# Kernel tuning notes

Measured on AMD Instinct MI355X. Metric: run time of the kernel, lower is better.

## Reference

```python
import jax, jax.numpy as jnp
import numpy as np

WINDOW_SIZE = 11
SIGMA = 1.5
C1 = 0.01 ** 2
C2 = 0.03 ** 2


def _gaussian_window(window_size, channel, dtype):
    coords = jnp.arange(window_size, dtype=jnp.float32) - window_size // 2
    g = jnp.exp(-(coords ** 2) / (2.0 * SIGMA ** 2))
    g = g / g.sum()
    w2d = jnp.outer(g, g)  # [K, K]
    # depthwise kernel: [channel, 1, K, K] (OIHW with feature_group_count=channel)
    return jnp.broadcast_to(w2d, (channel, 1, window_size, window_size)).astype(dtype)


def _dwconv(x, window, channel):
    pad = WINDOW_SIZE // 2
    return jax.lax.conv_general_dilated(
        x, window,
        window_strides=(1, 1),
        padding=[(pad, pad), (pad, pad)],
        dimension_numbers=('NCHW', 'OIHW', 'NCHW'),
        feature_group_count=channel,
    )


def _ssim(img1, img2):
    channel = img1.shape[1]
    window = _gaussian_window(WINDOW_SIZE, channel, img1.dtype)
    mu1 = _dwconv(img1, window, channel)
    mu2 = _dwconv(img2, window, channel)
    mu1_sq = mu1 * mu1
    mu2_sq = mu2 * mu2
    mu1_mu2 = mu1 * mu2
    sigma1_sq = _dwconv(img1 * img1, window, channel) - mu1_sq
    sigma2_sq = _dwconv(img2 * img2, window, channel) - mu2_sq
    sigma12 = _dwconv(img1 * img2, window, channel) - mu1_mu2
    ssim_map = ((2.0 * mu1_mu2 + C1) * (2.0 * sigma12 + C2)) / (
        (mu1_sq + mu2_sq + C1) * (sigma1_sq + sigma2_sq + C2))
    return ssim_map.mean()


def setup_inputs() -> dict:
    key = jax.random.key(0)
    k1, k2 = jax.random.split(key)
    img1 = jax.random.uniform(k1, (32, 3, 512, 512), dtype=jnp.float32)
    img2 = jax.random.uniform(k2, (32, 3, 512, 512), dtype=jnp.float32)
    return {"img1": img1, "img2": img2}


def reference(img1, img2):
    return _ssim(img1, img2)
```

## Files before the change

kernel.cpp:

```cpp
#include <hip/hip_runtime.h>
#include <cmath>

#define IMG_H 512
#define IMG_W 512
#define TH 32
#define TW 64
#define LDSW 75
#define NPLANES 96
#define NPIX 25165824.0

typedef float vf2 __attribute__((ext_vector_type(2)));

struct GaussW { float w[11]; };

__global__ __launch_bounds__(256, 4) void ssim_main(
    const float* __restrict__ img1, const float* __restrict__ img2,
    float* __restrict__ partials, GaussW gw, int use_atomic, float* __restrict__ out)
{
    __shared__ vf2 VAB[TH][LDSW];
    __shared__ vf2 VTS[TH][LDSW];
    __shared__ float wsum[4];

    const int tid = threadIdx.x;
    const int plane = blockIdx.z;
    const int tr0 = blockIdx.y * TH;
    const int tc0 = blockIdx.x * TW;
    const float* __restrict__ plane1 = img1 + ((size_t)plane << 18);
    const float* __restrict__ plane2 = img2 + ((size_t)plane << 18);

    {
        const int j = tid % 80;
        const int chunk = tid / 80;
        if (chunk < 3 && j < 74) {
            const int r0 = chunk * 11;
            const int gc = tc0 + j - 5;
            const float cmask = ((unsigned)gc < IMG_W) ? 1.f : 0.f;
            const int gcc = min(max(gc, 0), IMG_W - 1);

            vf2 aAB[11], aTS[11];

            #pragma unroll
            for (int ii = 0; ii < 21; ++ii) {
                const int gr = tr0 + r0 - 5 + ii;
                const float rmask = ((unsigned)gr < IMG_H) ? cmask : 0.f;
                const int grc = min(max(gr, 0), IMG_H - 1);
                const uint32_t idx = (uint32_t)(grc * IMG_W + gcc);
                const float a = plane1[idx] * rmask;
                const float b = plane2[idx] * rmask;
                const vf2 ab = { a, b };
                const vf2 pq = ab * ab;
                const vf2 ts = { pq.x + pq.y, a * b };
                #pragma unroll
                for (int o = 0; o < 11; ++o) {
                    if (o <= ii && ii <= o + 10) {
                        const float wt = gw.w[ii - o];
                        const vf2 wtv = { wt, wt };
                        if (ii == o) {
                            aAB[o] = wtv * ab;
                            aTS[o] = wtv * ts;
                        } else {
                            aAB[o] = __builtin_elementwise_fma(wtv, ab, aAB[o]);
                            aTS[o] = __builtin_elementwise_fma(wtv, ts, aTS[o]);
                        }
                    }
                }
            }
            #pragma unroll
            for (int o = 0; o < 11; ++o) {
                const int r = r0 + o;
                if (r0 + o < TH) {
                    VAB[r][j] = aAB[o];
                    VTS[r][j] = aTS[o];
                }
            }
        }
    }
    __syncthreads();

    float lsum = 0.f;
    {
        const int r = tid & 31;
        const int c0 = (tid >> 5) * 8;
        const vf2* __restrict__ bAB = &VAB[r][c0];
        const vf2* __restrict__ bTS = &VTS[r][c0];

        vf2 mAB[8], eTS[8];

        #pragma unroll
        for (int k = 0; k <= 17; ++k) {
            const vf2 vab = bAB[k];
            const vf2 vts = bTS[k];
            #pragma unroll
            for (int c = 0; c < 8; ++c) {
                if (k - 10 <= c && c <= k) {
                    const float wt = gw.w[k - c];
                    const vf2 wtv = { wt, wt };
                    if (k == c) {
                        mAB[c] = wtv * vab;
                        eTS[c] = wtv * vts;
                    } else {
                        mAB[c] = __builtin_elementwise_fma(wtv, vab, mAB[c]);
                        eTS[c] = __builtin_elementwise_fma(wtv, vts, eTS[c]);
                    }
                }
            }
        }
        #pragma unroll
        for (int c = 0; c < 8; ++c) {
            const float a1 = mAB[c].x, a2 = mAB[c].y;
            const float T  = eTS[c].x, S = eTS[c].y;
            const float h    = fmaf(a1, a1, a2 * a2);
            const float mu12 = a1 * a2;
            const float num  = fmaf(2.f, mu12, 0.0001f)
                             * fmaf(2.f, S - mu12, 0.0009f);
            const float den  = (h + 0.0001f) * ((T - h) + 0.0009f);
            lsum = fmaf(num, __builtin_amdgcn_rcpf(den), lsum);
        }
    }
    #pragma unroll
    for (int off = 32; off; off >>= 1) lsum += __shfl_down(lsum, off, 64);
    if ((tid & 63) == 0) wsum[tid >> 6] = lsum;
    __syncthreads();
    if (tid == 0) {
        const float bs = wsum[0] + wsum[1] + wsum[2] + wsum[3];
        if (use_atomic) {
            atomicAdd(out, bs * (float)(1.0 / NPIX));
        } else {
            const int bId = (blockIdx.z * gridDim.y + blockIdx.y) * gridDim.x + blockIdx.x;
            partials[bId] = bs;
        }
    }
}

__global__ __launch_bounds__(256) void ssim_reduce(
    const float* __restrict__ partials, int n, float* __restrict__ out)
{
    const int tid = threadIdx.x;
    double s = 0.0;
    for (int i = tid; i < n; i += 256) s += (double)partials[i];
    #pragma unroll
    for (int off = 32; off; off >>= 1) s += __shfl_down(s, off, 64);
    __shared__ double ws[4];
    if ((tid & 63) == 0) ws[tid >> 6] = s;
    __syncthreads();
    if (tid == 0) out[0] = (float)(((ws[0] + ws[1]) + (ws[2] + ws[3])) / NPIX);
}

extern "C" void kernel_launch(void* const* d_in, const int* in_sizes, int n_in,
                              void* d_out, int out_size, void* d_ws, size_t ws_size,
                              hipStream_t stream) {
    const float* img1 = (const float*)d_in[0];
    const float* img2 = (const float*)d_in[1];
    float* out = (float*)d_out;

    GaussW gw;
    {
        double g[11], sum = 0.0;
        for (int i = 0; i < 11; ++i) {
            const double c = (double)(i - 5);
            g[i] = std::exp(-(c * c) / 4.5);
            sum += g[i];
        }
        for (int i = 0; i < 11; ++i) gw.w[i] = (float)(g[i] / sum);
    }

    dim3 grid(IMG_W / TW, IMG_H / TH, NPLANES);
    const int nPart = grid.x * grid.y * grid.z;

    if (ws_size >= (size_t)nPart * sizeof(float)) {
        ssim_main<<<grid, 256, 0, stream>>>(img1, img2, (float*)d_ws, gw, 0, out);
        ssim_reduce<<<1, 256, 0, stream>>>((float*)d_ws, nPart, out);
    } else {
        hipMemsetAsync(d_out, 0, sizeof(float), stream);
        ssim_main<<<grid, 256, 0, stream>>>(img1, img2, nullptr, gw, 1, out);
    }
}
```

Baseline: 92.98 us.

## Reshape SSIM tiles to 16x118 with wave-row vertical pass

Changes the block tile from 32x64 to 16 rows by 118 output columns (128 staged columns, 5 blocks across), so the horizontal halo overhead per output shrinks and every thread does vertical-pass work. In the vertical pass each wave now handles 4 output rows over two 64-lane column passes, using row-wise branches instead of clamped masked loads. Columns beyond the image are masked at the end of the horizontal pass. The trade-off is more vertical halo per output (14 input rows per 4 outputs instead of 21 per 11), more redundant loads, and a ragged last column tile that wastes some work.

Result: slower. 210.9 us (+126.9%).

```diff
diff --git a/kernel.cpp b/kernel.cpp
--- a/kernel.cpp
+++ b/kernel.cpp
@@ -3,9 +3,11 @@
 
 #define IMG_H 512
 #define IMG_W 512
-#define TH 32
-#define TW 64
-#define LDSW 75
+#define TH 16
+#define TW 118
+#define SC 128
+#define LDSW 131
+#define GX 5
 #define NPLANES 96
 #define NPIX 25165824.0
 
@@ -22,6 +24,8 @@
     __shared__ float wsum[4];
 
     const int tid = threadIdx.x;
+    const int lane = tid & 63;
+    const int wid = __builtin_amdgcn_readfirstlane(tid >> 6);
     const int plane = blockIdx.z;
     const int tr0 = blockIdx.y * TH;
     const int tc0 = blockIdx.x * TW;
@@ -29,49 +33,45 @@
     const float* __restrict__ plane2 = img2 + ((size_t)plane << 18);
 
     {
-        const int j = tid % 80;
-        const int chunk = tid / 80;
-        if (chunk < 3 && j < 74) {
-            const int r0 = chunk * 11;
-            const int gc = tc0 + j - 5;
+        const int r0 = wid * 4;
+        #pragma unroll
+        for (int pass = 0; pass < 2; ++pass) {
+            const int sc = pass * 64 + lane;
+            const int gc = tc0 + sc - 5;
             const float cmask = ((unsigned)gc < IMG_W) ? 1.f : 0.f;
             const int gcc = min(max(gc, 0), IMG_W - 1);
 
-            vf2 aAB[11], aTS[11];
+            vf2 aAB[4], aTS[4];
+            #pragma unroll
+            for (int o = 0; o < 4; ++o) { aAB[o] = (vf2){0.f, 0.f}; aTS[o] = (vf2){0.f, 0.f}; }
 
             #pragma unroll
-            for (int ii = 0; ii < 21; ++ii) {
+            for (int ii = 0; ii < 14; ++ii) {
                 const int gr = tr0 + r0 - 5 + ii;
-                const float rmask = ((unsigned)gr < IMG_H) ? cmask : 0.f;
-                const int grc = min(max(gr, 0), IMG_H - 1);
-                const uint32_t idx = (uint32_t)(grc * IMG_W + gcc);
-                const float a = plane1[idx] * rmask;
-                const float b = plane2[idx] * rmask;
-                const vf2 ab = { a, b };
-                const vf2 pq = ab * ab;
-                const vf2 ts = { pq.x + pq.y, a * b };
-                #pragma unroll
-                for (int o = 0; o < 11; ++o) {
-                    if (o <= ii && ii <= o + 10) {
-                        const float wt = gw.w[ii - o];
-                        const vf2 wtv = { wt, wt };
-                        if (ii == o) {
-                            aAB[o] = wtv * ab;
-                            aTS[o] = wtv * ts;
-                        } else {
+                if ((unsigned)gr < (unsigned)IMG_H) {
+                    const float* __restrict__ r1 = plane1 + ((size_t)gr << 9);
+                    const float* __restrict__ r2 = plane2 + ((size_t)gr << 9);
+                    const float a = r1[gcc];
+                    const float b = r2[gcc];
+                    const vf2 ab = { a, b };
+                    const vf2 pq = ab * ab;
+                    const vf2 ts = { pq.x + pq.y, a * b };
+                    #pragma unroll
+                    for (int o = 0; o < 4; ++o) {
+                        if (o <= ii && ii <= o + 10) {
+                            const float wt = gw.w[ii - o];
+                            const vf2 wtv = { wt, wt };
                             aAB[o] = __builtin_elementwise_fma(wtv, ab, aAB[o]);
                             aTS[o] = __builtin_elementwise_fma(wtv, ts, aTS[o]);
                         }
                     }
                 }
             }
+            const vf2 cm = { cmask, cmask };
             #pragma unroll
-            for (int o = 0; o < 11; ++o) {
-                const int r = r0 + o;
-                if (r0 + o < TH) {
-                    VAB[r][j] = aAB[o];
-                    VTS[r][j] = aTS[o];
-                }
+            for (int o = 0; o < 4; ++o) {
+                VAB[r0 + o][sc] = aAB[o] * cm;
+                VTS[r0 + o][sc] = aTS[o] * cm;
             }
         }
     }
@@ -79,20 +79,20 @@
 
     float lsum = 0.f;
     {
-        const int r = tid & 31;
-        const int c0 = (tid >> 5) * 8;
+        const int r = tid & 15;
+        const int c0 = (tid >> 4) * 8;
         const vf2* __restrict__ bAB = &VAB[r][c0];
         const vf2* __restrict__ bTS = &VTS[r][c0];
+        const int cvalid = min(TW, IMG_W - tc0);
 
         vf2 mAB[8], eTS[8];
-
         #pragma unroll
         for (int k = 0; k <= 17; ++k) {
             const vf2 vab = bAB[k];
             const vf2 vts = bTS[k];
             #pragma unroll
             for (int c = 0; c < 8; ++c) {
-                if (k - 10 <= c && c <= k) {
+                if (c <= k && k <= c + 10) {
                     const float wt = gw.w[k - c];
                     const vf2 wtv = { wt, wt };
                     if (k == c) {
@@ -114,7 +114,8 @@
             const float num  = fmaf(2.f, mu12, 0.0001f)
                              * fmaf(2.f, S - mu12, 0.0009f);
             const float den  = (h + 0.0001f) * ((T - h) + 0.0009f);
-            lsum = fmaf(num, __builtin_amdgcn_rcpf(den), lsum);
+            const float val  = num * __builtin_amdgcn_rcpf(den);
+            lsum += (c0 + c < cvalid) ? val : 0.f;
         }
     }
     #pragma unroll
@@ -164,7 +165,7 @@
         for (int i = 0; i < 11; ++i) gw.w[i] = (float)(g[i] / sum);
     }
 
-    dim3 grid(IMG_W / TW, IMG_H / TH, NPLANES);
+    dim3 grid(GX, IMG_H / TH, NPLANES);
     const int nPart = grid.x * grid.y * grid.z;
 
     if (ws_size >= (size_t)nPart * sizeof(float)) {
```
